# Performance work log

Hardware: AMD Instinct MI355X
Metric: run time of the kernel (lower is better)

## Reference

```python
import jax, jax.numpy as jnp
import numpy as np

N_ATOMS = 8_000_000
N_REC = 2_000_000
N_POC = 500_000
N_CHAINS = 4


def setup_inputs() -> dict:
    key = jax.random.key(0)
    k1, k2, k3, k4 = jax.random.split(key, 4)
    # coordinates in nm, inside a ~5 nm box
    positions = jax.random.uniform(k1, (N_ATOMS, 3), dtype=jnp.float32) * 5.0
    box_vectors = jnp.diag(jnp.array([5.0, 5.0, 5.0], dtype=jnp.float32))
    # unique receptor atom indices into positions
    rec_indices = jax.random.permutation(k2, N_ATOMS)[:N_REC].astype(jnp.int32)
    # unique pocket indices INTO THE REC ARRAY (poc_pos = rec_pos[poc_indices])
    poc_indices = jax.random.permutation(k3, N_REC)[:N_POC].astype(jnp.int32)
    # contiguous chain assignment over rec atoms, all chains present in pocket
    chain_ids = ((jnp.arange(N_REC, dtype=jnp.int32) * N_CHAINS) // N_REC).astype(jnp.int32)
    poc_chain_ids = chain_ids[poc_indices]
    ref_poc = jax.random.uniform(k4, (N_POC, 3), dtype=jnp.float32) * 5.0
    k = jnp.float32(100.0)  # kJ/mol/nm^2
    return {
        "positions": positions, "box_vectors": box_vectors, "ref_poc": ref_poc,
        "k": k, "rec_indices": rec_indices, "poc_indices": poc_indices,
        "chain_ids": chain_ids, "poc_chain_ids": poc_chain_ids, "n_chains": N_CHAINS,
    }


def best_periodic_translation(pos1, pos2, box_vectors):
    # pos1, pos2: [C,3]; box_vectors: [3,3] (rows are lattice vectors)
    delta = pos2 - pos1
    inv = 1.0 / jnp.diag(box_vectors)
    s3 = jnp.round(delta[:, 2] * inv[2])
    delta = delta - s3[:, None] * box_vectors[2]
    s2 = jnp.round(delta[:, 1] * inv[1])
    delta = delta - s2[:, None] * box_vectors[1]
    s1 = jnp.round(delta[:, 0] * inv[0])
    return s1[:, None] * box_vectors[0] + s2[:, None] * box_vectors[1] + s3[:, None] * box_vectors[2]


def reference(positions, box_vectors, ref_poc, k, rec_indices, poc_indices, chain_ids, poc_chain_ids, n_chains):
    rec_pos = positions[rec_indices]  # [R,3]
    # Per-chain pocket COM. NOTE: original indexes global positions here
    # (positions[poc_chain_indices]), NOT rec_pos -- reproduced faithfully.
    poc_glob = positions[poc_indices]  # [P,3]
    counts = jax.ops.segment_sum(jnp.ones((poc_glob.shape[0],), poc_glob.dtype), poc_chain_ids, num_segments=n_chains)  # [C]
    poc_com = jax.ops.segment_sum(poc_glob, poc_chain_ids, num_segments=n_chains) / counts[:, None]  # [C,3]
    ref_com = jax.ops.segment_sum(ref_poc, poc_chain_ids, num_segments=n_chains) / counts[:, None]  # [C,3]
    best_t = best_periodic_translation(poc_com, ref_com, box_vectors)  # [C,3]
    rec_pos = rec_pos + best_t[chain_ids]  # translate each chain into the reference image

    poc_pos = rec_pos[poc_indices]  # [P,3]
    rec_origin = jnp.mean(rec_pos, axis=0)
    rec_centered = rec_pos - rec_origin
    r_sq = jnp.sum(rec_centered ** 2, axis=1)  # [R]
    F = jnp.zeros_like(rec_pos).at[poc_indices].set(-2.0 * k * (poc_pos - ref_poc))
    F_mean = jnp.mean(F, axis=0)
    torque = jnp.cross(rec_centered, F)
    torque_mean = jnp.mean(torque, axis=0)
    F_rot = jnp.cross(torque_mean[None], rec_centered) / r_sq[:, None]
    F_final = jnp.zeros_like(positions).at[rec_indices].set(F_mean + F_rot)
    return (jnp.float32(0.0), F_final)
```

## Files before the change

### kernel.cpp

```cpp
#include <hip/hip_runtime.h>


typedef unsigned int uint32;
typedef unsigned char uchar;

#define MAXC 16
#define W_BT 0
#define W_O 48
#define W_FM 52
#define W_TM 56
#define W_ACC 64

#define GCOUNT_OFF 4096
#define REC_OFF 8192
#define NB 512
#define BSH 14
#define BUCKET_ATOMS (1 << BSH)
#define CAP 5120
#define INV8_OFF (REC_OFF + NB * CAP * 4)

#define PB 512
#define RB 512
#define K1_KPT 16
#define K1_CHUNK (256 * K1_KPT)

struct PartSh { uint32 hist[NB]; uint32 curs[NB]; uint32 base[NB]; };
struct PocSh  { float red[4][43]; float accL[3 + MAXC * 10]; };
union ShU { PartSh part; PocSh poc; };

__device__ inline float waveSum(float v) {
#pragma unroll
  for (int off = 32; off > 0; off >>= 1) v += __shfl_down(v, off, 64);
  return v;
}

__global__ __launch_bounds__(256) void k_fused(
    const float* __restrict__ pos, const float* __restrict__ ref_poc,
    const int* __restrict__ rec_idx, const int* __restrict__ cid,
    const int* __restrict__ poc_idx, const int* __restrict__ poc_cid,
    const int* __restrict__ ncp, int R, int P,
    uint32* __restrict__ gcount, uint32* __restrict__ grecords,
    float* __restrict__ ws) {
  const int tid = threadIdx.x;
  const int bid = blockIdx.x;
  __shared__ ShU sh;
  const int C = ncp[0];

  if (bid < PB) {
    const int gsz = PB * 256;
    if (C <= 4) {
      float vals[43];
#pragma unroll
      for (int v = 0; v < 43; ++v) vals[v] = 0.f;
      for (int rb = bid * 256 + tid; rb < P; rb += 4 * gsz) {
        int rr[4], i2[4], c2[4], ri[4];
        float g[4][3], p[4][3], rf[4][3];
#pragma unroll
        for (int q = 0; q < 4; ++q) {
          int r = rb + q * gsz;
          rr[q] = (r < P) ? r : -1;
        }
#pragma unroll
        for (int q = 0; q < 4; ++q) {
          int r = (rr[q] < 0) ? 0 : rr[q];
          i2[q] = poc_idx[r];
          c2[q] = poc_cid[r];
        }
#pragma unroll
        for (int q = 0; q < 4; ++q) {
          ri[q] = rec_idx[i2[q]];
          g[q][0] = pos[3 * i2[q] + 0];
          g[q][1] = pos[3 * i2[q] + 1];
          g[q][2] = pos[3 * i2[q] + 2];
        }
#pragma unroll
        for (int q = 0; q < 4; ++q) {
          int r = (rr[q] < 0) ? 0 : rr[q];
          p[q][0] = pos[3 * ri[q] + 0];
          p[q][1] = pos[3 * ri[q] + 1];
          p[q][2] = pos[3 * ri[q] + 2];
          rf[q][0] = ref_poc[3 * r + 0];
          rf[q][1] = ref_poc[3 * r + 1];
          rf[q][2] = ref_poc[3 * r + 2];
        }
#pragma unroll
        for (int q = 0; q < 4; ++q) {
          if (rr[q] >= 0) {
            vals[0] += p[q][1] * rf[q][2] - p[q][2] * rf[q][1];
            vals[1] += p[q][2] * rf[q][0] - p[q][0] * rf[q][2];
            vals[2] += p[q][0] * rf[q][1] - p[q][1] * rf[q][0];
#pragma unroll
            for (int cc = 0; cc < 4; ++cc) {
              bool m = (c2[q] == cc);
              float* a = &vals[3 + cc * 10];
              a[0] += m ? g[q][0] : 0.f; a[1] += m ? g[q][1] : 0.f;
              a[2] += m ? g[q][2] : 0.f;
              a[3] += m ? rf[q][0] : 0.f; a[4] += m ? rf[q][1] : 0.f;
              a[5] += m ? rf[q][2] : 0.f;
              a[6] += m ? p[q][0] : 0.f; a[7] += m ? p[q][1] : 0.f;
              a[8] += m ? p[q][2] : 0.f;
              a[9] += m ? 1.f : 0.f;
            }
          }
        }
      }
      const int wid = tid >> 6;
#pragma unroll
      for (int v = 0; v < 43; ++v) {
        float s = waveSum(vals[v]);
        if ((tid & 63) == 0) sh.poc.red[wid][v] = s;
      }
      __syncthreads();
      for (int t = tid; t < 43; t += 256)
        atomicAdd(&ws[W_ACC + 19 + t], sh.poc.red[0][t] + sh.poc.red[1][t] +
                                       sh.poc.red[2][t] + sh.poc.red[3][t]);
    } else {
      float* accL = sh.poc.accL;
      for (int t = tid; t < 3 + MAXC * 10; t += 256) accL[t] = 0.f;
      __syncthreads();
      for (int r = bid * 256 + tid; r < P; r += PB * 256) {
        int i2 = poc_idx[r];
        int c2 = poc_cid[r];
        int ri = rec_idx[i2];
        float gx = pos[3 * i2 + 0], gy = pos[3 * i2 + 1], gz = pos[3 * i2 + 2];
        float px = pos[3 * ri + 0], py = pos[3 * ri + 1], pz = pos[3 * ri + 2];
        float rx = ref_poc[3 * r + 0], ry = ref_poc[3 * r + 1], rz = ref_poc[3 * r + 2];
        atomicAdd(&accL[0], py * rz - pz * ry);
        atomicAdd(&accL[1], pz * rx - px * rz);
        atomicAdd(&accL[2], px * ry - py * rx);
        float* a = &accL[3 + c2 * 10];
        atomicAdd(&a[0], gx); atomicAdd(&a[1], gy); atomicAdd(&a[2], gz);
        atomicAdd(&a[3], rx); atomicAdd(&a[4], ry); atomicAdd(&a[5], rz);
        atomicAdd(&a[6], px); atomicAdd(&a[7], py); atomicAdd(&a[8], pz);
        atomicAdd(&a[9], 1.f);
      }
      __syncthreads();
      for (int t = tid; t < 3 + MAXC * 10; t += 256)
        if (accL[t] != 0.f) atomicAdd(&ws[W_ACC + 19 + t], accL[t]);
    }
  } else {
    const int pb = bid - PB;
    uint32* hist = sh.part.hist;
    uint32* curs = sh.part.curs;
    uint32* base = sh.part.base;
    for (int r0 = pb * K1_CHUNK; r0 < R; r0 += RB * K1_CHUNK) {
      int cnt = R - r0; if (cnt > K1_CHUNK) cnt = K1_CHUNK;
      for (int t = tid; t < NB; t += 256) { hist[t] = 0u; curs[t] = 0u; }
      __syncthreads();
      uint32 enc[K1_KPT];
#pragma unroll
      for (int j = 0; j < K1_KPT; ++j) {
        int t = tid + j * 256;
        uint32 e = 0xFFFFFFFFu;
        if (t < cnt) {
          uint32 idx = (uint32)rec_idx[r0 + t];
          uint32 c = (uint32)cid[r0 + t] & 255u;
          e = (idx << 8) | c;
          atomicAdd(&hist[idx >> BSH], 1u);
        }
        enc[j] = e;
      }
      __syncthreads();
      for (int t = tid; t < NB; t += 256) {
        uint32 h = hist[t];
        base[t] = h ? atomicAdd(&gcount[t], h) : 0u;
      }
      __syncthreads();
#pragma unroll
      for (int j = 0; j < K1_KPT; ++j) {
        uint32 e = enc[j];
        if (e != 0xFFFFFFFFu) {
          uint32 b = e >> (8 + BSH);
          uint32 slot = base[b] + atomicAdd(&curs[b], 1u);
          if (slot < CAP) grecords[b * CAP + slot] = e;
        }
      }
      __syncthreads();
    }
  }
}

__global__ __launch_bounds__(256) void k_bucket_build(
    const float4* __restrict__ pos4, const int* __restrict__ ncp,
    const uint32* __restrict__ gcount, const uint32* __restrict__ grecords,
    int N, uchar* __restrict__ inv8, float* __restrict__ ws) {
  const int tid = threadIdx.x;
  const int b = blockIdx.x;
  const int a0 = b << BSH;
  if (a0 >= N) return;
  int natoms = N - a0; if (natoms > BUCKET_ATOMS) natoms = BUCKET_ATOMS;

  __shared__ uchar map_[BUCKET_ATOMS];
  __shared__ float cnt16[MAXC];
  uint4* m16 = (uint4*)map_;
  uint4 ff; ff.x = ff.y = ff.z = ff.w = 0xFFFFFFFFu;
  for (int t = tid; t < BUCKET_ATOMS / 16; t += 256) m16[t] = ff;
  const int C = ncp[0];
  if (C > 4) for (int t = tid; t < MAXC; t += 256) cnt16[t] = 0.f;
  __syncthreads();

  int n = (int)gcount[b]; if (n > CAP) n = CAP;
  float c0 = 0.f, c1 = 0.f, c2 = 0.f, c3 = 0.f;
  for (int t = tid; t < n; t += 256) {
    uint32 e = grecords[b * CAP + t];
    uint32 ia = (e >> 8) & (BUCKET_ATOMS - 1);
    uint32 c = e & 255u;
    map_[ia] = (uchar)c;
    if (C <= 4) {
      c0 += (c == 0u) ? 1.f : 0.f;
      c1 += (c == 1u) ? 1.f : 0.f;
      c2 += (c == 2u) ? 1.f : 0.f;
      c3 += (c == 3u) ? 1.f : 0.f;
    } else {
      atomicAdd(&cnt16[c], 1.f);
    }
  }
  __syncthreads();

  uchar* dst = inv8 + a0;
  if (natoms == BUCKET_ATOMS) {
    uint4* d16 = (uint4*)dst;
    for (int t = tid; t < BUCKET_ATOMS / 16; t += 256) d16[t] = m16[t];
  } else {
    for (int t = tid; t < natoms; t += 256) dst[t] = map_[t];
  }

  float sx = 0.f, sy = 0.f, sz = 0.f;
  int ngf = natoms >> 2;
  const uchar4* m4 = (const uchar4*)map_;
  int g0 = a0 >> 2;
  for (int g = tid; g < ngf; g += 256) {
    float4 p0 = pos4[3 * (g0 + g) + 0];
    float4 p1 = pos4[3 * (g0 + g) + 1];
    float4 p2 = pos4[3 * (g0 + g) + 2];
    uchar4 m = m4[g];
    if (m.x != 255) { sx += p0.x; sy += p0.y; sz += p0.z; }
    if (m.y != 255) { sx += p0.w; sy += p1.x; sz += p1.y; }
    if (m.z != 255) { sx += p1.z; sy += p1.w; sz += p2.x; }
    if (m.w != 255) { sx += p2.y; sy += p2.z; sz += p2.w; }
  }
  int tb = natoms & 3;
  if (tid < tb) {
    int a = a0 + (ngf << 2) + tid;
    const float* pf = (const float*)pos4;
    if (map_[(ngf << 2) + tid] != 255) {
      sx += pf[3 * a]; sy += pf[3 * a + 1]; sz += pf[3 * a + 2];
    }
  }

  __shared__ float red[4][7];
  float vv[7] = {sx, sy, sz, c0, c1, c2, c3};
  const int wid = tid >> 6;
#pragma unroll
  for (int v = 0; v < 7; ++v) {
    float s = waveSum(vv[v]);
    if ((tid & 63) == 0) red[wid][v] = s;
  }
  __syncthreads();
  if (tid < 7) {
    float s = red[0][tid] + red[1][tid] + red[2][tid] + red[3][tid];
    atomicAdd(&ws[W_ACC + tid], s);
  }
  if (C > 4 && tid < C) atomicAdd(&ws[W_ACC + 3 + tid], cnt16[tid]);
}

__global__ void k_finalize(const float* __restrict__ box,
                           const float* __restrict__ kp,
                           const int* __restrict__ ncp,
                           int R, float* __restrict__ ws) {
  __shared__ float tot[192];
  const int C = ncp[0];
  for (int t = threadIdx.x; t < 192; t += blockDim.x) tot[t] = ws[W_ACC + t];
  __syncthreads();
  if (threadIdx.x != 0) return;
  const float kk = kp[0];
  const float Rf = (float)R;
  const float* xp = &tot[19];
  float inv0 = 1.f / box[0], inv1 = 1.f / box[4], inv2 = 1.f / box[8];
  float ox = tot[0], oy = tot[1], oz = tot[2];
  float Fx = 0, Fy = 0, Fz = 0;
  float T1x = 0, T1y = 0, T1z = 0, T2x = 0, T2y = 0, T2z = 0;
  for (int c = 0; c < C; ++c) {
    float nrec = tot[3 + c];
    const float* a = &tot[22 + c * 10];
    float np = a[9];
    float invn = 1.f / np;
    float pcx = a[0] * invn, pcy = a[1] * invn, pcz = a[2] * invn;
    float rcx = a[3] * invn, rcy = a[4] * invn, rcz = a[5] * invn;
    float dx = rcx - pcx, dy = rcy - pcy, dz = rcz - pcz;
    float s3 = rintf(dz * inv2);
    dx -= s3 * box[6]; dy -= s3 * box[7]; dz -= s3 * box[8];
    float s2 = rintf(dy * inv1);
    dx -= s2 * box[3]; dy -= s2 * box[4]; dz -= s2 * box[5];
    float s1 = rintf(dx * inv0);
    float btx = s1 * box[0] + s2 * box[3] + s3 * box[6];
    float bty = s1 * box[1] + s2 * box[4] + s3 * box[7];
    float btz = s1 * box[2] + s2 * box[5] + s3 * box[8];
    ws[W_BT + c * 3 + 0] = btx;
    ws[W_BT + c * 3 + 1] = bty;
    ws[W_BT + c * 3 + 2] = btz;
    ox += nrec * btx; oy += nrec * bty; oz += nrec * btz;
    float SFx = -2.f * kk * (a[6] + np * btx - a[3]);
    float SFy = -2.f * kk * (a[7] + np * bty - a[4]);
    float SFz = -2.f * kk * (a[8] + np * btz - a[5]);
    Fx += SFx; Fy += SFy; Fz += SFz;
    T1x += a[7] * btz - a[8] * bty;
    T1y += a[8] * btx - a[6] * btz;
    T1z += a[6] * bty - a[7] * btx;
    T2x += bty * SFz - btz * SFy;
    T2y += btz * SFx - btx * SFz;
    T2z += btx * SFy - bty * SFx;
  }
  ox /= Rf; oy /= Rf; oz /= Rf;
  float Tx = 2.f * kk * xp[0] - 2.f * kk * T1x + T2x - (oy * Fz - oz * Fy);
  float Ty = 2.f * kk * xp[1] - 2.f * kk * T1y + T2y - (oz * Fx - ox * Fz);
  float Tz = 2.f * kk * xp[2] - 2.f * kk * T1z + T2z - (ox * Fy - oy * Fx);
  ws[W_O + 0] = ox; ws[W_O + 1] = oy; ws[W_O + 2] = oz;
  ws[W_FM + 0] = Fx / Rf; ws[W_FM + 1] = Fy / Rf; ws[W_FM + 2] = Fz / Rf;
  ws[W_TM + 0] = Tx / Rf; ws[W_TM + 1] = Ty / Rf; ws[W_TM + 2] = Tz / Rf;
}

__global__ __launch_bounds__(256) void k_final_dense(
    const float* __restrict__ pos, const uchar* __restrict__ inv8,
    int N, const float* __restrict__ ws, float* __restrict__ out) {
  __shared__ float stage[3328];
  __shared__ float sc[64];
  const int tid = threadIdx.x;
  if (tid < 64) sc[tid] = ws[tid];
  const int t0 = blockIdx.x * 1024;
  int nat = N - t0; if (nat > 1024) nat = 1024;
  const int nfl = nat * 3;

  if (nat == 1024) {
    const float4* src4 = (const float4*)(pos + 3 * t0);
#pragma unroll
    for (int kk = 0; kk < 3; ++kk) {
      int v4 = tid + kk * 256;
      float4 p = src4[v4];
      int idx = 4 * v4 + v4 / 3;
      stage[idx + 0] = p.x; stage[idx + 1] = p.y;
      stage[idx + 2] = p.z; stage[idx + 3] = p.w;
    }
  } else {
    for (int k = tid; k < nfl; k += 256)
      stage[k + (int)((unsigned)k / 12u)] = pos[3 * t0 + k];
  }
  __syncthreads();

  float ox = sc[W_O + 0], oy = sc[W_O + 1], oz = sc[W_O + 2];
  float fmx = sc[W_FM + 0], fmy = sc[W_FM + 1], fmz = sc[W_FM + 2];
  float tmx = sc[W_TM + 0], tmy = sc[W_TM + 1], tmz = sc[W_TM + 2];

  uchar mc[4];
  if (nat == 1024) {
    uchar4 m = ((const uchar4*)(inv8 + t0))[tid];
    mc[0] = m.x; mc[1] = m.y; mc[2] = m.z; mc[3] = m.w;
  } else {
#pragma unroll
    for (int q = 0; q < 4; ++q) {
      int la = 4 * tid + q;
      mc[q] = (la < nat) ? inv8[t0 + la] : (uchar)255;
    }
  }
#pragma unroll
  for (int q = 0; q < 4; ++q) {
    int la = 4 * tid + q;
    if (la < nat) {
      float* s = &stage[13 * tid + 3 * q];
      float fx = 0.f, fy = 0.f, fz = 0.f;
      int c = mc[q];
      if (c != 255) {
        float cx = s[0] + sc[W_BT + 3 * c + 0] - ox;
        float cy = s[1] + sc[W_BT + 3 * c + 1] - oy;
        float cz = s[2] + sc[W_BT + 3 * c + 2] - oz;
        float inv = 1.f / (cx * cx + cy * cy + cz * cz);
        fx = fmx + (tmy * cz - tmz * cy) * inv;
        fy = fmy + (tmz * cx - tmx * cz) * inv;
        fz = fmz + (tmx * cy - tmy * cx) * inv;
      }
      s[0] = fx; s[1] = fy; s[2] = fz;
    }
  }
  __syncthreads();

  if (blockIdx.x == 0 && tid == 0) out[0] = 0.f;
  float* ob = out + 1 + 3 * t0;
  if (nat == 1024) {
#pragma unroll
    for (int kk = 0; kk < 3; ++kk) {
      int j = tid + kk * 256;
      if (j < 767) {
        int k = 3 + 4 * j;
        float4 v;
        v.x = stage[k + k / 12];
        v.y = stage[(k + 1) + (k + 1) / 12];
        v.z = stage[(k + 2) + (k + 2) / 12];
        v.w = stage[(k + 3) + (k + 3) / 12];
        *(float4*)(ob + k) = v;
      }
    }
    if (tid < 3) ob[tid] = stage[tid];
    if (tid == 3) ob[3071] = stage[3071 + 3071 / 12];
  } else {
    for (int k = tid; k < nfl; k += 256)
      ob[k] = stage[k + (int)((unsigned)k / 12u)];
  }
}

extern "C" void kernel_launch(void* const* d_in, const int* in_sizes, int n_in,
                              void* d_out, int out_size, void* d_ws, size_t ws_size,
                              hipStream_t stream) {
  const float* pos     = (const float*)d_in[0];
  const float* box     = (const float*)d_in[1];
  const float* ref_poc = (const float*)d_in[2];
  const float* kp      = (const float*)d_in[3];
  const int* rec_idx   = (const int*)d_in[4];
  const int* poc_idx   = (const int*)d_in[5];
  const int* cid       = (const int*)d_in[6];
  const int* poc_cid   = (const int*)d_in[7];
  const int* ncp       = (const int*)d_in[8];
  float* out = (float*)d_out;
  float* ws  = (float*)d_ws;
  uint32* gcount   = (uint32*)((char*)d_ws + GCOUNT_OFF);
  uint32* grecords = (uint32*)((char*)d_ws + REC_OFF);
  uchar* inv8      = (uchar*)d_ws + INV8_OFF;

  const int N = in_sizes[0] / 3;
  const int R = in_sizes[4];
  const int P = in_sizes[5];

  hipMemsetAsync(d_ws, 0, 8192, stream);

  k_fused<<<PB + RB, 256, 0, stream>>>(pos, ref_poc, rec_idx, cid, poc_idx,
                                       poc_cid, ncp, R, P, gcount, grecords, ws);
  k_bucket_build<<<NB, 256, 0, stream>>>((const float4*)pos, ncp, gcount,
                                         grecords, N, inv8, ws);
  k_finalize<<<1, 256, 0, stream>>>(box, kp, ncp, R, ws);
  int gF = (N + 1023) / 1024;
  k_final_dense<<<gF, 256, 0, stream>>>(pos, inv8, N, ws, out);
}
```

Baseline: 267.4 us.

## Fuse all stages into one persistent kernel with atomic task queue and spin-waits

Replaces the four separate kernel launches with a single persistent kernel of fixed grid. Blocks pull tasks from a global atomic counter in dependency order: pocket reduction, partitioning, bucket build, finalize, then dense output tiles. Cross-stage dependencies are enforced with release/acquire counters and bounded spin-waits. This removes launch gaps and tail bubbles between stages, but adds spin overhead, relies on all blocks making forward progress, and caps occupancy through launch bounds.

```diff
diff --git a/kernel.cpp b/kernel.cpp
--- a/kernel.cpp
+++ b/kernel.cpp
@@ -10,6 +10,13 @@
 #define W_FM 52
 #define W_TM 56
 #define W_ACC 64
+
+#define CUR_OFF   3584
+#define DCUR_OFF  3712
+#define POCD_OFF  3840
+#define PARTD_OFF 3848
+#define BCD_OFF   3856
+#define FZD_OFF   3864
 
 #define GCOUNT_OFF 4096
 #define REC_OFF 8192
@@ -19,14 +26,20 @@
 #define CAP 5120
 #define INV8_OFF (REC_OFF + NB * CAP * 4)
 
-#define PB 512
-#define RB 512
+#define TPOC 512
 #define K1_KPT 16
 #define K1_CHUNK (256 * K1_KPT)
+#define DBATCH 4
+#define GRID 1024
+
+#define SPIN_MAX (1 << 20)
 
 struct PartSh { uint32 hist[NB]; uint32 curs[NB]; uint32 base[NB]; };
 struct PocSh  { float red[4][43]; float accL[3 + MAXC * 10]; };
-union ShU { PartSh part; PocSh poc; };
+struct MapSh  { uchar map_[BUCKET_ATOMS]; };
+struct StageSh{ float stage[3328]; };
+union ShU { PartSh part; PocSh poc; MapSh map; StageSh st; };
+struct MiscSh { float red7[4][7]; float sc[64]; float cnt16[MAXC]; float tot[192]; };
 
 __device__ inline float waveSum(float v) {
 #pragma unroll
@@ -34,376 +47,427 @@
   return v;
 }
 
-__global__ __launch_bounds__(256) void k_fused(
+__device__ inline uint32 aload(const uint32* p) {
+  return __hip_atomic_load(p, __ATOMIC_ACQUIRE, __HIP_MEMORY_SCOPE_AGENT);
+}
+__device__ inline void adone(uint32* p) {
+  __threadfence();
+  __hip_atomic_fetch_add(p, 1u, __ATOMIC_RELEASE, __HIP_MEMORY_SCOPE_AGENT);
+}
+
+__global__ __launch_bounds__(256, 4) void k_all(
     const float* __restrict__ pos, const float* __restrict__ ref_poc,
     const int* __restrict__ rec_idx, const int* __restrict__ cid,
     const int* __restrict__ poc_idx, const int* __restrict__ poc_cid,
-    const int* __restrict__ ncp, int R, int P,
+    const int* __restrict__ ncp, const float* __restrict__ box,
+    const float* __restrict__ kp, int R, int P, int N,
     uint32* __restrict__ gcount, uint32* __restrict__ grecords,
-    float* __restrict__ ws) {
+    uchar* __restrict__ inv8, float* __restrict__ ws,
+    float* __restrict__ out,
+    uint32* __restrict__ qcur, uint32* __restrict__ dcur,
+    uint32* __restrict__ pocd, uint32* __restrict__ partd,
+    uint32* __restrict__ bcd, uint32* __restrict__ fzd) {
+  __shared__ ShU sh;
+  __shared__ MiscSh ms;
+  __shared__ int shTask;
+  __shared__ int shSeen;
   const int tid = threadIdx.x;
-  const int bid = blockIdx.x;
-  __shared__ ShU sh;
   const int C = ncp[0];
-
-  if (bid < PB) {
-    const int gsz = PB * 256;
-    if (C <= 4) {
-      float vals[43];
-#pragma unroll
-      for (int v = 0; v < 43; ++v) vals[v] = 0.f;
-      for (int rb = bid * 256 + tid; rb < P; rb += 4 * gsz) {
-        int rr[4], i2[4], c2[4], ri[4];
-        float g[4][3], p[4][3], rf[4][3];
-#pragma unroll
-        for (int q = 0; q < 4; ++q) {
-          int r = rb + q * gsz;
-          rr[q] = (r < P) ? r : -1;
-        }
-#pragma unroll
-        for (int q = 0; q < 4; ++q) {
-          int r = (rr[q] < 0) ? 0 : rr[q];
-          i2[q] = poc_idx[r];
-          c2[q] = poc_cid[r];
-        }
-#pragma unroll
-        for (int q = 0; q < 4; ++q) {
-          ri[q] = rec_idx[i2[q]];
-          g[q][0] = pos[3 * i2[q] + 0];
-          g[q][1] = pos[3 * i2[q] + 1];
-          g[q][2] = pos[3 * i2[q] + 2];
-        }
-#pragma unroll
-        for (int q = 0; q < 4; ++q) {
-          int r = (rr[q] < 0) ? 0 : rr[q];
-          p[q][0] = pos[3 * ri[q] + 0];
-          p[q][1] = pos[3 * ri[q] + 1];
-          p[q][2] = pos[3 * ri[q] + 2];
-          rf[q][0] = ref_poc[3 * r + 0];
-          rf[q][1] = ref_poc[3 * r + 1];
-          rf[q][2] = ref_poc[3 * r + 2];
-        }
-#pragma unroll
-        for (int q = 0; q < 4; ++q) {
-          if (rr[q] >= 0) {
-            vals[0] += p[q][1] * rf[q][2] - p[q][2] * rf[q][1];
-            vals[1] += p[q][2] * rf[q][0] - p[q][0] * rf[q][2];
-            vals[2] += p[q][0] * rf[q][1] - p[q][1] * rf[q][0];
-#pragma unroll
-            for (int cc = 0; cc < 4; ++cc) {
-              bool m = (c2[q] == cc);
-              float* a = &vals[3 + cc * 10];
-              a[0] += m ? g[q][0] : 0.f; a[1] += m ? g[q][1] : 0.f;
-              a[2] += m ? g[q][2] : 0.f;
-              a[3] += m ? rf[q][0] : 0.f; a[4] += m ? rf[q][1] : 0.f;
-              a[5] += m ? rf[q][2] : 0.f;
-              a[6] += m ? p[q][0] : 0.f; a[7] += m ? p[q][1] : 0.f;
-              a[8] += m ? p[q][2] : 0.f;
-              a[9] += m ? 1.f : 0.f;
+  const int NCHUNK = (R + K1_CHUNK - 1) / K1_CHUNK;
+  const int T_PART_END = TPOC + NCHUNK;
+  const int T_BC_END = T_PART_END + NB;
+  const int T_FZ_END = T_BC_END + 1;
+  const int ntiles = (N + 1023) >> 10;
+  if (tid == 0) shSeen = 0;
+
+  for (;;) {
+    __syncthreads();
+    if (tid == 0) shTask = (int)atomicAdd(qcur, 1u);
+    __syncthreads();
+    const int t = shTask;
+    if (t >= T_FZ_END) break;
+
+    if (t < TPOC) {
+      const int gsz = TPOC * 256;
+      if (C <= 4) {
+        float vals[43];
+#pragma unroll
+        for (int v = 0; v < 43; ++v) vals[v] = 0.f;
+        for (int rb = t * 256 + tid; rb < P; rb += 4 * gsz) {
+          int rr[4], i2[4], c2[4], ri[4];
+          float g[4][3], p[4][3], rf[4][3];
+#pragma unroll
+          for (int q = 0; q < 4; ++q) {
+            int r = rb + q * gsz;
+            rr[q] = (r < P) ? r : -1;
+          }
+#pragma unroll
+          for (int q = 0; q < 4; ++q) {
+            int r = (rr[q] < 0) ? 0 : rr[q];
+            i2[q] = poc_idx[r];
+            c2[q] = poc_cid[r];
+          }
+#pragma unroll
+          for (int q = 0; q < 4; ++q) {
+            ri[q] = rec_idx[i2[q]];
+            g[q][0] = pos[3 * i2[q] + 0];
+            g[q][1] = pos[3 * i2[q] + 1];
+            g[q][2] = pos[3 * i2[q] + 2];
+          }
+#pragma unroll
+          for (int q = 0; q < 4; ++q) {
+            int r = (rr[q] < 0) ? 0 : rr[q];
+            p[q][0] = pos[3 * ri[q] + 0];
+            p[q][1] = pos[3 * ri[q] + 1];
+            p[q][2] = pos[3 * ri[q] + 2];
+            rf[q][0] = ref_poc[3 * r + 0];
+            rf[q][1] = ref_poc[3 * r + 1];
+            rf[q][2] = ref_poc[3 * r + 2];
+          }
+#pragma unroll
+          for (int q = 0; q < 4; ++q) {
+            if (rr[q] >= 0) {
+              vals[0] += p[q][1] * rf[q][2] - p[q][2] * rf[q][1];
+              vals[1] += p[q][2] * rf[q][0] - p[q][0] * rf[q][2];
+              vals[2] += p[q][0] * rf[q][1] - p[q][1] * rf[q][0];
+#pragma unroll
+              for (int cc = 0; cc < 4; ++cc) {
+                bool m = (c2[q] == cc);
+                float* a = &vals[3 + cc * 10];
+                a[0] += m ? g[q][0] : 0.f; a[1] += m ? g[q][1] : 0.f;
+                a[2] += m ? g[q][2] : 0.f;
+                a[3] += m ? rf[q][0] : 0.f; a[4] += m ? rf[q][1] : 0.f;
+                a[5] += m ? rf[q][2] : 0.f;
+                a[6] += m ? p[q][0] : 0.f; a[7] += m ? p[q][1] : 0.f;
+                a[8] += m ? p[q][2] : 0.f;
+                a[9] += m ? 1.f : 0.f;
+              }
             }
           }
         }
-      }
-      const int wid = tid >> 6;
-#pragma unroll
-      for (int v = 0; v < 43; ++v) {
-        float s = waveSum(vals[v]);
-        if ((tid & 63) == 0) sh.poc.red[wid][v] = s;
-      }
-      __syncthreads();
-      for (int t = tid; t < 43; t += 256)
-        atomicAdd(&ws[W_ACC + 19 + t], sh.poc.red[0][t] + sh.poc.red[1][t] +
-                                       sh.poc.red[2][t] + sh.poc.red[3][t]);
-    } else {
-      float* accL = sh.poc.accL;
-      for (int t = tid; t < 3 + MAXC * 10; t += 256) accL[t] = 0.f;
-      __syncthreads();
-      for (int r = bid * 256 + tid; r < P; r += PB * 256) {
-        int i2 = poc_idx[r];
-        int c2 = poc_cid[r];
-        int ri = rec_idx[i2];
-        float gx = pos[3 * i2 + 0], gy = pos[3 * i2 + 1], gz = pos[3 * i2 + 2];
-        float px = pos[3 * ri + 0], py = pos[3 * ri + 1], pz = pos[3 * ri + 2];
-        float rx = ref_poc[3 * r + 0], ry = ref_poc[3 * r + 1], rz = ref_poc[3 * r + 2];
-        atomicAdd(&accL[0], py * rz - pz * ry);
-        atomicAdd(&accL[1], pz * rx - px * rz);
-        atomicAdd(&accL[2], px * ry - py * rx);
-        float* a = &accL[3 + c2 * 10];
-        atomicAdd(&a[0], gx); atomicAdd(&a[1], gy); atomicAdd(&a[2], gz);
-        atomicAdd(&a[3], rx); atomicAdd(&a[4], ry); atomicAdd(&a[5], rz);
-        atomicAdd(&a[6], px); atomicAdd(&a[7], py); atomicAdd(&a[8], pz);
-        atomicAdd(&a[9], 1.f);
-      }
-      __syncthreads();
-      for (int t = tid; t < 3 + MAXC * 10; t += 256)
-        if (accL[t] != 0.f) atomicAdd(&ws[W_ACC + 19 + t], accL[t]);
-    }
-  } else {
-    const int pb = bid - PB;
-    uint32* hist = sh.part.hist;
-    uint32* curs = sh.part.curs;
-    uint32* base = sh.part.base;
-    for (int r0 = pb * K1_CHUNK; r0 < R; r0 += RB * K1_CHUNK) {
+        const int wid = tid >> 6;
+#pragma unroll
+        for (int v = 0; v < 43; ++v) {
+          float s = waveSum(vals[v]);
+          if ((tid & 63) == 0) sh.poc.red[wid][v] = s;
+        }
+        __syncthreads();
+        for (int s = tid; s < 43; s += 256)
+          atomicAdd(&ws[W_ACC + 19 + s], sh.poc.red[0][s] + sh.poc.red[1][s] +
+                                         sh.poc.red[2][s] + sh.poc.red[3][s]);
+      } else {
+        float* accL = sh.poc.accL;
+        for (int s = tid; s < 3 + MAXC * 10; s += 256) accL[s] = 0.f;
+        __syncthreads();
+        for (int r = t * 256 + tid; r < P; r += TPOC * 256) {
+          int i2 = poc_idx[r];
+          int c2 = poc_cid[r];
+          int ri = rec_idx[i2];
+          float gx = pos[3 * i2 + 0], gy = pos[3 * i2 + 1], gz = pos[3 * i2 + 2];
+          float px = pos[3 * ri + 0], py = pos[3 * ri + 1], pz = pos[3 * ri + 2];
+          float rx = ref_poc[3 * r + 0], ry = ref_poc[3 * r + 1], rz = ref_poc[3 * r + 2];
+          atomicAdd(&accL[0], py * rz - pz * ry);
+          atomicAdd(&accL[1], pz * rx - px * rz);
+          atomicAdd(&accL[2], px * ry - py * rx);
+          float* a = &accL[3 + c2 * 10];
+          atomicAdd(&a[0], gx); atomicAdd(&a[1], gy); atomicAdd(&a[2], gz);
+          atomicAdd(&a[3], rx); atomicAdd(&a[4], ry); atomicAdd(&a[5], rz);
+          atomicAdd(&a[6], px); atomicAdd(&a[7], py); atomicAdd(&a[8], pz);
+          atomicAdd(&a[9], 1.f);
+        }
+        __syncthreads();
+        for (int s = tid; s < 3 + MAXC * 10; s += 256)
+          if (accL[s] != 0.f) atomicAdd(&ws[W_ACC + 19 + s], accL[s]);
+      }
+      if (tid == 0) adone(pocd);
+
+    } else if (t < T_PART_END) {
+      const int j = t - TPOC;
+      const int r0 = j * K1_CHUNK;
       int cnt = R - r0; if (cnt > K1_CHUNK) cnt = K1_CHUNK;
-      for (int t = tid; t < NB; t += 256) { hist[t] = 0u; curs[t] = 0u; }
+      uint32* hist = sh.part.hist;
+      uint32* curs = sh.part.curs;
+      uint32* base = sh.part.base;
+      for (int s = tid; s < NB; s += 256) { hist[s] = 0u; curs[s] = 0u; }
       __syncthreads();
       uint32 enc[K1_KPT];
 #pragma unroll
-      for (int j = 0; j < K1_KPT; ++j) {
-        int t = tid + j * 256;
+      for (int jj = 0; jj < K1_KPT; ++jj) {
+        int s = tid + jj * 256;
         uint32 e = 0xFFFFFFFFu;
-        if (t < cnt) {
-          uint32 idx = (uint32)rec_idx[r0 + t];
-          uint32 c = (uint32)cid[r0 + t] & 255u;
+        if (s < cnt) {
+          uint32 idx = (uint32)rec_idx[r0 + s];
+          uint32 c = (uint32)cid[r0 + s] & 255u;
           e = (idx << 8) | c;
           atomicAdd(&hist[idx >> BSH], 1u);
         }
-        enc[j] = e;
-      }
-      __syncthreads();
-      for (int t = tid; t < NB; t += 256) {
-        uint32 h = hist[t];
-        base[t] = h ? atomicAdd(&gcount[t], h) : 0u;
-      }
-      __syncthreads();
-#pragma unroll
-      for (int j = 0; j < K1_KPT; ++j) {
-        uint32 e = enc[j];
+        enc[jj] = e;
+      }
+      __syncthreads();
+      for (int s = tid; s < NB; s += 256) {
+        uint32 h = hist[s];
+        base[s] = h ? atomicAdd(&gcount[s], h) : 0u;
+      }
+      __syncthreads();
+#pragma unroll
+      for (int jj = 0; jj < K1_KPT; ++jj) {
+        uint32 e = enc[jj];
         if (e != 0xFFFFFFFFu) {
           uint32 b = e >> (8 + BSH);
           uint32 slot = base[b] + atomicAdd(&curs[b], 1u);
           if (slot < CAP) grecords[b * CAP + slot] = e;
         }
       }
-      __syncthreads();
+      if (tid == 0) adone(partd);
+
+    } else if (t < T_BC_END) {
+      if (!(shSeen & 1)) {
+        if (tid == 0) {
+          for (int it = 0; it < SPIN_MAX; ++it) {
+            if (aload(partd) >= (uint32)NCHUNK) break;
+            __builtin_amdgcn_s_sleep(2);
+          }
+          shSeen |= 1;
+        }
+        __syncthreads();
+        __threadfence();
+      }
+      const int b = t - T_PART_END;
+      const int a0 = b << BSH;
+      if (a0 < N) {
+        int natoms = N - a0; if (natoms > BUCKET_ATOMS) natoms = BUCKET_ATOMS;
+        uchar* map_ = sh.map.map_;
+        uint4* m16 = (uint4*)map_;
+        uint4 ff; ff.x = ff.y = ff.z = ff.w = 0xFFFFFFFFu;
+        for (int s = tid; s < BUCKET_ATOMS / 16; s += 256) m16[s] = ff;
+        if (C > 4) for (int s = tid; s < MAXC; s += 256) ms.cnt16[s] = 0.f;
+        __syncthreads();
+        int n = (int)gcount[b]; if (n > CAP) n = CAP;
+        float c0 = 0.f, c1 = 0.f, c2 = 0.f, c3 = 0.f;
+        for (int s = tid; s < n; s += 256) {
+          uint32 e = grecords[b * CAP + s];
+          uint32 ia = (e >> 8) & (BUCKET_ATOMS - 1);
+          uint32 c = e & 255u;
+          map_[ia] = (uchar)c;
+          if (C <= 4) {
+            c0 += (c == 0u) ? 1.f : 0.f;
+            c1 += (c == 1u) ? 1.f : 0.f;
+            c2 += (c == 2u) ? 1.f : 0.f;
+            c3 += (c == 3u) ? 1.f : 0.f;
+          } else {
+            atomicAdd(&ms.cnt16[c], 1.f);
+          }
+        }
+        __syncthreads();
+        uchar* dst = inv8 + a0;
+        if (natoms == BUCKET_ATOMS) {
+          uint4* d16 = (uint4*)dst;
+          for (int s = tid; s < BUCKET_ATOMS / 16; s += 256) d16[s] = m16[s];
+        } else {
+          for (int s = tid; s < natoms; s += 256) dst[s] = map_[s];
+        }
+        float sx = 0.f, sy = 0.f, sz = 0.f;
+        int ngf = natoms >> 2;
+        const uchar4* m4 = (const uchar4*)map_;
+        const float4* pos4 = (const float4*)pos;
+        int g0 = a0 >> 2;
+        for (int g = tid; g < ngf; g += 256) {
+          float4 p0 = pos4[3 * (g0 + g) + 0];
+          float4 p1 = pos4[3 * (g0 + g) + 1];
+          float4 p2 = pos4[3 * (g0 + g) + 2];
+          uchar4 m = m4[g];
+          if (m.x != 255) { sx += p0.x; sy += p0.y; sz += p0.z; }
+          if (m.y != 255) { sx += p0.w; sy += p1.x; sz += p1.y; }
+          if (m.z != 255) { sx += p1.z; sy += p1.w; sz += p2.x; }
+          if (m.w != 255) { sx += p2.y; sy += p2.z; sz += p2.w; }
+        }
+        int tb = natoms & 3;
+        if (tid < tb) {
+          int a = a0 + (ngf << 2) + tid;
+          const float* pf = (const float*)pos4;
+          if (map_[(ngf << 2) + tid] != 255) {
+            sx += pf[3 * a]; sy += pf[3 * a + 1]; sz += pf[3 * a + 2];
+          }
+        }
+        float vv[7] = {sx, sy, sz, c0, c1, c2, c3};
+        const int wid = tid >> 6;
+#pragma unroll
+        for (int v = 0; v < 7; ++v) {
+          float s = waveSum(vv[v]);
+          if ((tid & 63) == 0) ms.red7[wid][v] = s;
+        }
+        __syncthreads();
+        if (tid < 7) {
+          float s = ms.red7[0][tid] + ms.red7[1][tid] +
+                    ms.red7[2][tid] + ms.red7[3][tid];
+          atomicAdd(&ws[W_ACC + tid], s);
+        }
+        if (C > 4 && tid < C) atomicAdd(&ws[W_ACC + 3 + tid], ms.cnt16[tid]);
+      }
+      if (tid == 0) adone(bcd);
+
+    } else {
+      if (tid == 0) {
+        for (int it = 0; it < SPIN_MAX; ++it) {
+          if (aload(pocd) >= (uint32)TPOC && aload(bcd) >= (uint32)NB) break;
+          __builtin_amdgcn_s_sleep(2);
+        }
+      }
+      __syncthreads();
+      __threadfence();
+      for (int s = tid; s < 192; s += 256) ms.tot[s] = ws[W_ACC + s];
+      __syncthreads();
+      if (tid == 0) {
+        float* tot = ms.tot;
+        const float kk = kp[0];
+        const float Rf = (float)R;
+        const float* xp = &tot[19];
+        float inv0 = 1.f / box[0], inv1 = 1.f / box[4], inv2 = 1.f / box[8];
+        float ox = tot[0], oy = tot[1], oz = tot[2];
+        float Fx = 0, Fy = 0, Fz = 0;
+        float T1x = 0, T1y = 0, T1z = 0, T2x = 0, T2y = 0, T2z = 0;
+        for (int c = 0; c < C; ++c) {
+          float nrec = tot[3 + c];
+          const float* a = &tot[22 + c * 10];
+          float np = a[9];
+          float invn = 1.f / np;
+          float pcx = a[0] * invn, pcy = a[1] * invn, pcz = a[2] * invn;
+          float rcx = a[3] * invn, rcy = a[4] * invn, rcz = a[5] * invn;
+          float dx = rcx - pcx, dy = rcy - pcy, dz = rcz - pcz;
+          float s3 = rintf(dz * inv2);
+          dx -= s3 * box[6]; dy -= s3 * box[7]; dz -= s3 * box[8];
+          float s2 = rintf(dy * inv1);
+          dx -= s2 * box[3]; dy -= s2 * box[4]; dz -= s2 * box[5];
+          float s1 = rintf(dx * inv0);
+          float btx = s1 * box[0] + s2 * box[3] + s3 * box[6];
+          float bty = s1 * box[1] + s2 * box[4] + s3 * box[7];
+          float btz = s1 * box[2] + s2 * box[5] + s3 * box[8];
+          ws[W_BT + c * 3 + 0] = btx;
+          ws[W_BT + c * 3 + 1] = bty;
+          ws[W_BT + c * 3 + 2] = btz;
+          ox += nrec * btx; oy += nrec * bty; oz += nrec * btz;
+          float SFx = -2.f * kk * (a[6] + np * btx - a[3]);
+          float SFy = -2.f * kk * (a[7] + np * bty - a[4]);
+          float SFz = -2.f * kk * (a[8] + np * btz - a[5]);
+          Fx += SFx; Fy += SFy; Fz += SFz;
+          T1x += a[7] * btz - a[8] * bty;
+          T1y += a[8] * btx - a[6] * btz;
+          T1z += a[6] * bty - a[7] * btx;
+          T2x += bty * SFz - btz * SFy;
+          T2y += btz * SFx - btx * SFz;
+          T2z += btx * SFy - bty * SFx;
+        }
+        ox /= Rf; oy /= Rf; oz /= Rf;
+        float Tx = 2.f * kk * xp[0] - 2.f * kk * T1x + T2x - (oy * Fz - oz * Fy);
+        float Ty = 2.f * kk * xp[1] - 2.f * kk * T1y + T2y - (oz * Fx - ox * Fz);
+        float Tz = 2.f * kk * xp[2] - 2.f * kk * T1z + T2z - (ox * Fy - oy * Fx);
+        ws[W_O + 0] = ox; ws[W_O + 1] = oy; ws[W_O + 2] = oz;
+        ws[W_FM + 0] = Fx / Rf; ws[W_FM + 1] = Fy / Rf; ws[W_FM + 2] = Fz / Rf;
+        ws[W_TM + 0] = Tx / Rf; ws[W_TM + 1] = Ty / Rf; ws[W_TM + 2] = Tz / Rf;
+        adone(fzd);
+      }
     }
   }
-}
-
-__global__ __launch_bounds__(256) void k_bucket_build(
-    const float4* __restrict__ pos4, const int* __restrict__ ncp,
-    const uint32* __restrict__ gcount, const uint32* __restrict__ grecords,
-    int N, uchar* __restrict__ inv8, float* __restrict__ ws) {
-  const int tid = threadIdx.x;
-  const int b = blockIdx.x;
-  const int a0 = b << BSH;
-  if (a0 >= N) return;
-  int natoms = N - a0; if (natoms > BUCKET_ATOMS) natoms = BUCKET_ATOMS;
-
-  __shared__ uchar map_[BUCKET_ATOMS];
-  __shared__ float cnt16[MAXC];
-  uint4* m16 = (uint4*)map_;
-  uint4 ff; ff.x = ff.y = ff.z = ff.w = 0xFFFFFFFFu;
-  for (int t = tid; t < BUCKET_ATOMS / 16; t += 256) m16[t] = ff;
-  const int C = ncp[0];
-  if (C > 4) for (int t = tid; t < MAXC; t += 256) cnt16[t] = 0.f;
-  __syncthreads();
-
-  int n = (int)gcount[b]; if (n > CAP) n = CAP;
-  float c0 = 0.f, c1 = 0.f, c2 = 0.f, c3 = 0.f;
-  for (int t = tid; t < n; t += 256) {
-    uint32 e = grecords[b * CAP + t];
-    uint32 ia = (e >> 8) & (BUCKET_ATOMS - 1);
-    uint32 c = e & 255u;
-    map_[ia] = (uchar)c;
-    if (C <= 4) {
-      c0 += (c == 0u) ? 1.f : 0.f;
-      c1 += (c == 1u) ? 1.f : 0.f;
-      c2 += (c == 2u) ? 1.f : 0.f;
-      c3 += (c == 3u) ? 1.f : 0.f;
-    } else {
-      atomicAdd(&cnt16[c], 1.f);
+
+  if (tid == 0) {
+    for (int it = 0; it < SPIN_MAX; ++it) {
+      if (aload(fzd) >= 1u) break;
+      __builtin_amdgcn_s_sleep(2);
     }
   }
   __syncthreads();
-
-  uchar* dst = inv8 + a0;
-  if (natoms == BUCKET_ATOMS) {
-    uint4* d16 = (uint4*)dst;
-    for (int t = tid; t < BUCKET_ATOMS / 16; t += 256) d16[t] = m16[t];
-  } else {
-    for (int t = tid; t < natoms; t += 256) dst[t] = map_[t];
-  }
-
-  float sx = 0.f, sy = 0.f, sz = 0.f;
-  int ngf = natoms >> 2;
-  const uchar4* m4 = (const uchar4*)map_;
-  int g0 = a0 >> 2;
-  for (int g = tid; g < ngf; g += 256) {
-    float4 p0 = pos4[3 * (g0 + g) + 0];
-    float4 p1 = pos4[3 * (g0 + g) + 1];
-    float4 p2 = pos4[3 * (g0 + g) + 2];
-    uchar4 m = m4[g];
-    if (m.x != 255) { sx += p0.x; sy += p0.y; sz += p0.z; }
-    if (m.y != 255) { sx += p0.w; sy += p1.x; sz += p1.y; }
-    if (m.z != 255) { sx += p1.z; sy += p1.w; sz += p2.x; }
-    if (m.w != 255) { sx += p2.y; sy += p2.z; sz += p2.w; }
-  }
-  int tb = natoms & 3;
-  if (tid < tb) {
-    int a = a0 + (ngf << 2) + tid;
-    const float* pf = (const float*)pos4;
-    if (map_[(ngf << 2) + tid] != 255) {
-      sx += pf[3 * a]; sy += pf[3 * a + 1]; sz += pf[3 * a + 2];
+  __threadfence();
+  if (tid < 64) ms.sc[tid] = ws[tid];
+  __syncthreads();
+  float* sc = ms.sc;
+  const float ox = sc[W_O + 0], oy = sc[W_O + 1], oz = sc[W_O + 2];
+  const float fmx = sc[W_FM + 0], fmy = sc[W_FM + 1], fmz = sc[W_FM + 2];
+  const float tmx = sc[W_TM + 0], tmy = sc[W_TM + 1], tmz = sc[W_TM + 2];
+
+  for (;;) {
+    if (tid == 0) shTask = (int)atomicAdd(dcur, (uint32)DBATCH);
+    __syncthreads();
+    const int tb = shTask;
+    if (tb >= ntiles) break;
+    const int te = (tb + DBATCH < ntiles) ? (tb + DBATCH) : ntiles;
+    for (int tile = tb; tile < te; ++tile) {
+      const int t0 = tile << 10;
+      int nat = N - t0; if (nat > 1024) nat = 1024;
+      const int nfl = nat * 3;
+      float* stage = sh.st.stage;
+
+      if (nat == 1024) {
+        const float4* src4 = (const float4*)(pos + 3 * t0);
+#pragma unroll
+        for (int kk = 0; kk < 3; ++kk) {
+          int v4 = tid + kk * 256;
+          float4 p = src4[v4];
+          int idx = 4 * v4 + v4 / 3;
+          stage[idx + 0] = p.x; stage[idx + 1] = p.y;
+          stage[idx + 2] = p.z; stage[idx + 3] = p.w;
+        }
+      } else {
+        for (int k = tid; k < nfl; k += 256)
+          stage[k + (int)((unsigned)k / 12u)] = pos[3 * t0 + k];
+      }
+      __syncthreads();
+
+      uchar mc[4];
+      if (nat == 1024) {
+        uchar4 m = ((const uchar4*)(inv8 + t0))[tid];
+        mc[0] = m.x; mc[1] = m.y; mc[2] = m.z; mc[3] = m.w;
+      } else {
+#pragma unroll
+        for (int q = 0; q < 4; ++q) {
+          int la = 4 * tid + q;
+          mc[q] = (la < nat) ? inv8[t0 + la] : (uchar)255;
+        }
+      }
+#pragma unroll
+      for (int q = 0; q < 4; ++q) {
+        int la = 4 * tid + q;
+        if (la < nat) {
+          float* s = &stage[13 * tid + 3 * q];
+          float fx = 0.f, fy = 0.f, fz = 0.f;
+          int c = mc[q];
+          if (c != 255) {
+            float cx = s[0] + sc[W_BT + 3 * c + 0] - ox;
+            float cy = s[1] + sc[W_BT + 3 * c + 1] - oy;
+            float cz = s[2] + sc[W_BT + 3 * c + 2] - oz;
+            float inv = 1.f / (cx * cx + cy * cy + cz * cz);
+            fx = fmx + (tmy * cz - tmz * cy) * inv;
+            fy = fmy + (tmz * cx - tmx * cz) * inv;
+            fz = fmz + (tmx * cy - tmy * cx) * inv;
+          }
+          s[0] = fx; s[1] = fy; s[2] = fz;
+        }
+      }
+      __syncthreads();
+
+      if (tile == 0 && tid == 0) out[0] = 0.f;
+      float* ob = out + 1 + 3 * t0;
+      if (nat == 1024) {
+#pragma unroll
+        for (int kk = 0; kk < 3; ++kk) {
+          int j = tid + kk * 256;
+          if (j < 767) {
+            int k = 3 + 4 * j;
+            float4 v;
+            v.x = stage[k + k / 12];
+            v.y = stage[(k + 1) + (k + 1) / 12];
+            v.z = stage[(k + 2) + (k + 2) / 12];
+            v.w = stage[(k + 3) + (k + 3) / 12];
+            *(float4*)(ob + k) = v;
+          }
+        }
+        if (tid < 3) ob[tid] = stage[tid];
+        if (tid == 3) ob[3071] = stage[3071 + 3071 / 12];
+      } else {
+        for (int k = tid; k < nfl; k += 256)
+          ob[k] = stage[k + (int)((unsigned)k / 12u)];
+      }
+      __syncthreads();
     }
-  }
-
-  __shared__ float red[4][7];
-  float vv[7] = {sx, sy, sz, c0, c1, c2, c3};
-  const int wid = tid >> 6;
-#pragma unroll
-  for (int v = 0; v < 7; ++v) {
-    float s = waveSum(vv[v]);
-    if ((tid & 63) == 0) red[wid][v] = s;
-  }
-  __syncthreads();
-  if (tid < 7) {
-    float s = red[0][tid] + red[1][tid] + red[2][tid] + red[3][tid];
-    atomicAdd(&ws[W_ACC + tid], s);
-  }
-  if (C > 4 && tid < C) atomicAdd(&ws[W_ACC + 3 + tid], cnt16[tid]);
-}
-
-__global__ void k_finalize(const float* __restrict__ box,
-                           const float* __restrict__ kp,
-                           const int* __restrict__ ncp,
-                           int R, float* __restrict__ ws) {
-  __shared__ float tot[192];
-  const int C = ncp[0];
-  for (int t = threadIdx.x; t < 192; t += blockDim.x) tot[t] = ws[W_ACC + t];
-  __syncthreads();
-  if (threadIdx.x != 0) return;
-  const float kk = kp[0];
-  const float Rf = (float)R;
-  const float* xp = &tot[19];
-  float inv0 = 1.f / box[0], inv1 = 1.f / box[4], inv2 = 1.f / box[8];
-  float ox = tot[0], oy = tot[1], oz = tot[2];
-  float Fx = 0, Fy = 0, Fz = 0;
-  float T1x = 0, T1y = 0, T1z = 0, T2x = 0, T2y = 0, T2z = 0;
-  for (int c = 0; c < C; ++c) {
-    float nrec = tot[3 + c];
-    const float* a = &tot[22 + c * 10];
-    float np = a[9];
-    float invn = 1.f / np;
-    float pcx = a[0] * invn, pcy = a[1] * invn, pcz = a[2] * invn;
-    float rcx = a[3] * invn, rcy = a[4] * invn, rcz = a[5] * invn;
-    float dx = rcx - pcx, dy = rcy - pcy, dz = rcz - pcz;
-    float s3 = rintf(dz * inv2);
-    dx -= s3 * box[6]; dy -= s3 * box[7]; dz -= s3 * box[8];
-    float s2 = rintf(dy * inv1);
-    dx -= s2 * box[3]; dy -= s2 * box[4]; dz -= s2 * box[5];
-    float s1 = rintf(dx * inv0);
-    float btx = s1 * box[0] + s2 * box[3] + s3 * box[6];
-    float bty = s1 * box[1] + s2 * box[4] + s3 * box[7];
-    float btz = s1 * box[2] + s2 * box[5] + s3 * box[8];
-    ws[W_BT + c * 3 + 0] = btx;
-    ws[W_BT + c * 3 + 1] = bty;
-    ws[W_BT + c * 3 + 2] = btz;
-    ox += nrec * btx; oy += nrec * bty; oz += nrec * btz;
-    float SFx = -2.f * kk * (a[6] + np * btx - a[3]);
-    float SFy = -2.f * kk * (a[7] + np * bty - a[4]);
-    float SFz = -2.f * kk * (a[8] + np * btz - a[5]);
-    Fx += SFx; Fy += SFy; Fz += SFz;
-    T1x += a[7] * btz - a[8] * bty;
-    T1y += a[8] * btx - a[6] * btz;
-    T1z += a[6] * bty - a[7] * btx;
-    T2x += bty * SFz - btz * SFy;
-    T2y += btz * SFx - btx * SFz;
-    T2z += btx * SFy - bty * SFx;
-  }
-  ox /= Rf; oy /= Rf; oz /= Rf;
-  float Tx = 2.f * kk * xp[0] - 2.f * kk * T1x + T2x - (oy * Fz - oz * Fy);
-  float Ty = 2.f * kk * xp[1] - 2.f * kk * T1y + T2y - (oz * Fx - ox * Fz);
-  float Tz = 2.f * kk * xp[2] - 2.f * kk * T1z + T2z - (ox * Fy - oy * Fx);
-  ws[W_O + 0] = ox; ws[W_O + 1] = oy; ws[W_O + 2] = oz;
-  ws[W_FM + 0] = Fx / Rf; ws[W_FM + 1] = Fy / Rf; ws[W_FM + 2] = Fz / Rf;
-  ws[W_TM + 0] = Tx / Rf; ws[W_TM + 1] = Ty / Rf; ws[W_TM + 2] = Tz / Rf;
-}
-
-__global__ __launch_bounds__(256) void k_final_dense(
-    const float* __restrict__ pos, const uchar* __restrict__ inv8,
-    int N, const float* __restrict__ ws, float* __restrict__ out) {
-  __shared__ float stage[3328];
-  __shared__ float sc[64];
-  const int tid = threadIdx.x;
-  if (tid < 64) sc[tid] = ws[tid];
-  const int t0 = blockIdx.x * 1024;
-  int nat = N - t0; if (nat > 1024) nat = 1024;
-  const int nfl = nat * 3;
-
-  if (nat == 1024) {
-    const float4* src4 = (const float4*)(pos + 3 * t0);
-#pragma unroll
-    for (int kk = 0; kk < 3; ++kk) {
-      int v4 = tid + kk * 256;
-      float4 p = src4[v4];
-      int idx = 4 * v4 + v4 / 3;
-      stage[idx + 0] = p.x; stage[idx + 1] = p.y;
-      stage[idx + 2] = p.z; stage[idx + 3] = p.w;
-    }
-  } else {
-    for (int k = tid; k < nfl; k += 256)
-      stage[k + (int)((unsigned)k / 12u)] = pos[3 * t0 + k];
-  }
-  __syncthreads();
-
-  float ox = sc[W_O + 0], oy = sc[W_O + 1], oz = sc[W_O + 2];
-  float fmx = sc[W_FM + 0], fmy = sc[W_FM + 1], fmz = sc[W_FM + 2];
-  float tmx = sc[W_TM + 0], tmy = sc[W_TM + 1], tmz = sc[W_TM + 2];
-
-  uchar mc[4];
-  if (nat == 1024) {
-    uchar4 m = ((const uchar4*)(inv8 + t0))[tid];
-    mc[0] = m.x; mc[1] = m.y; mc[2] = m.z; mc[3] = m.w;
-  } else {
-#pragma unroll
-    for (int q = 0; q < 4; ++q) {
-      int la = 4 * tid + q;
-      mc[q] = (la < nat) ? inv8[t0 + la] : (uchar)255;
-    }
-  }
-#pragma unroll
-  for (int q = 0; q < 4; ++q) {
-    int la = 4 * tid + q;
-    if (la < nat) {
-      float* s = &stage[13 * tid + 3 * q];
-      float fx = 0.f, fy = 0.f, fz = 0.f;
-      int c = mc[q];
-      if (c != 255) {
-        float cx = s[0] + sc[W_BT + 3 * c + 0] - ox;
-        float cy = s[1] + sc[W_BT + 3 * c + 1] - oy;
-        float cz = s[2] + sc[W_BT + 3 * c + 2] - oz;
-        float inv = 1.f / (cx * cx + cy * cy + cz * cz);
-        fx = fmx + (tmy * cz - tmz * cy) * inv;
-        fy = fmy + (tmz * cx - tmx * cz) * inv;
-        fz = fmz + (tmx * cy - tmy * cx) * inv;
-      }
-      s[0] = fx; s[1] = fy; s[2] = fz;
-    }
-  }
-  __syncthreads();
-
-  if (blockIdx.x == 0 && tid == 0) out[0] = 0.f;
-  float* ob = out + 1 + 3 * t0;
-  if (nat == 1024) {
-#pragma unroll
-    for (int kk = 0; kk < 3; ++kk) {
-      int j = tid + kk * 256;
-      if (j < 767) {
-        int k = 3 + 4 * j;
-        float4 v;
-        v.x = stage[k + k / 12];
-        v.y = stage[(k + 1) + (k + 1) / 12];
-        v.z = stage[(k + 2) + (k + 2) / 12];
-        v.w = stage[(k + 3) + (k + 3) / 12];
-        *(float4*)(ob + k) = v;
-      }
-    }
-    if (tid < 3) ob[tid] = stage[tid];
-    if (tid == 3) ob[3071] = stage[3071 + 3071 / 12];
-  } else {
-    for (int k = tid; k < nfl; k += 256)
-      ob[k] = stage[k + (int)((unsigned)k / 12u)];
   }
 }
 
@@ -421,9 +485,15 @@
   const int* ncp       = (const int*)d_in[8];
   float* out = (float*)d_out;
   float* ws  = (float*)d_ws;
+  uint32* qcur     = (uint32*)((char*)d_ws + CUR_OFF);
+  uint32* dcur     = (uint32*)((char*)d_ws + DCUR_OFF);
+  uint32* pocd     = (uint32*)((char*)d_ws + POCD_OFF);
+  uint32* partd    = (uint32*)((char*)d_ws + PARTD_OFF);
+  uint32* bcd      = (uint32*)((char*)d_ws + BCD_OFF);
+  uint32* fzd      = (uint32*)((char*)d_ws + FZD_OFF);
   uint32* gcount   = (uint32*)((char*)d_ws + GCOUNT_OFF);
   uint32* grecords = (uint32*)((char*)d_ws + REC_OFF);
-  uchar* inv8      = (uchar*)d_ws + INV8_OFF;
+  uchar*  inv8     = (uchar*)d_ws + INV8_OFF;
 
   const int N = in_sizes[0] / 3;
   const int R = in_sizes[4];
@@ -431,11 +501,8 @@
 
   hipMemsetAsync(d_ws, 0, 8192, stream);
 
-  k_fused<<<PB + RB, 256, 0, stream>>>(pos, ref_poc, rec_idx, cid, poc_idx,
-                                       poc_cid, ncp, R, P, gcount, grecords, ws);
-  k_bucket_build<<<NB, 256, 0, stream>>>((const float4*)pos, ncp, gcount,
-                                         grecords, N, inv8, ws);
-  k_finalize<<<1, 256, 0, stream>>>(box, kp, ncp, R, ws);
-  int gF = (N + 1023) / 1024;
-  k_final_dense<<<gF, 256, 0, stream>>>(pos, inv8, N, ws, out);
+  k_all<<<GRID, 256, 0, stream>>>(
+      pos, ref_poc, rec_idx, cid, poc_idx, poc_cid, ncp, box, kp,
+      R, P, N, gcount, grecords, inv8, ws, out,
+      qcur, dcur, pocd, partd, bcd, fzd);
 }
```

Result: slower. 874.8 us (+227.2%).
